# Optimization experiments

Hardware: AMD Instinct MI355X
Metric: run time of the kernel (lower is better)

## Reference

```python
import jax, jax.numpy as jnp
import numpy as np

B, L, D, H, F = 4, 1024, 1024, 16, 4096
HD = D // H
EPS = 1e-5


def _xavier(key, shape):
    fan_in, fan_out = shape[1], shape[0]
    a = np.sqrt(6.0 / (fan_in + fan_out)).astype(np.float32)
    return jax.random.uniform(key, shape, jnp.float32, -a, a)


def setup_inputs() -> dict:
    key = jax.random.key(0)
    ks = jax.random.split(key, 8)
    x = jax.random.normal(ks[0], (B, L, D), jnp.float32)
    attn_mask = jnp.zeros((L, L), jnp.float32)
    return {
        "x": x,
        "attn_mask": attn_mask,
        "in_proj_w": _xavier(ks[1], (3 * D, D)),
        "in_proj_b": jnp.zeros((3 * D,), jnp.float32),
        "out_proj_w": _xavier(ks[2], (D, D)),
        "out_proj_b": jnp.zeros((D,), jnp.float32),
        "lin1_w": _xavier(ks[3], (F, D)),
        "lin1_b": jnp.zeros((F,), jnp.float32),
        "lin2_w": _xavier(ks[4], (D, F)),
        "lin2_b": jnp.zeros((D,), jnp.float32),
        "ln1_g": jnp.ones((D,), jnp.float32),
        "ln1_b": jnp.zeros((D,), jnp.float32),
        "ln2_g": jnp.ones((D,), jnp.float32),
        "ln2_b": jnp.zeros((D,), jnp.float32),
    }


def _layernorm(x, g, b):
    mu = jnp.mean(x, axis=-1, keepdims=True)
    var = jnp.mean(jnp.square(x - mu), axis=-1, keepdims=True)
    return (x - mu) * jax.lax.rsqrt(var + EPS) * g + b


def reference(x, attn_mask, in_proj_w, in_proj_b, out_proj_w, out_proj_b,
              lin1_w, lin1_b, lin2_w, lin2_b, ln1_g, ln1_b, ln2_g, ln2_b):
    # --- self-attention (need_weights=True, average_attn_weights=False) ---
    qkv = x @ in_proj_w.T + in_proj_b          # [B,L,3D]
    q, k, v = jnp.split(qkv, 3, axis=-1)
    q = q.reshape(B, L, H, HD).transpose(0, 2, 1, 3)  # [B,H,L,hd]
    k = k.reshape(B, L, H, HD).transpose(0, 2, 1, 3)
    v = v.reshape(B, L, H, HD).transpose(0, 2, 1, 3)
    scores = jnp.einsum('bhqd,bhkd->bhqk', q, k) / np.sqrt(HD).astype(np.float32)
    scores = scores + attn_mask                # additive [L,L] mask
    attn_w = jax.nn.softmax(scores, axis=-1)   # [B,H,L,L] materialized weights
    ctx = jnp.einsum('bhqk,bhkd->bhqd', attn_w, v)
    ctx = ctx.transpose(0, 2, 1, 3).reshape(B, L, D)
    attn_out = ctx @ out_proj_w.T + out_proj_b
    # --- norm_first=False residual blocks ---
    x = _layernorm(x + attn_out, ln1_g, ln1_b)
    ff = jax.nn.relu(x @ lin1_w.T + lin1_b) @ lin2_w.T + lin2_b
    x = _layernorm(x + ff, ln2_g, ln2_b)
    return (x, attn_w)
```

## Files before the change

kernel.cpp:

```cpp
#include <hip/hip_runtime.h>

#define Bq 4
#define Lq 1024
#define Dq 1024
#define Hq 16
#define HDq 64
#define Fq 4096
#define Mq (Bq*Lq)

typedef unsigned short u16;
using short8  = __attribute__((ext_vector_type(8))) short;
using floatx4 = __attribute__((ext_vector_type(4))) float;

__device__ __forceinline__ float b2f(u16 u) {
  union { unsigned int i; float f; } v; v.i = ((unsigned int)u) << 16; return v.f;
}
__device__ __forceinline__ u16 f2b(float f) {
  union { float f; unsigned int i; } v; v.f = f;
  unsigned int x = v.i;
  unsigned int r = x + 0x7fffu + ((x >> 16) & 1u);
  return (u16)(r >> 16);
}

__device__ __forceinline__ void split2(float v, u16& hi, u16& lo) {
  hi = f2b(v);
  lo = f2b(v - b2f(hi));
}

__device__ __forceinline__ void gl_lds16(const u16* g, u16* l) {
  __builtin_amdgcn_global_load_lds(
      (const __attribute__((address_space(1))) void*)g,
      (__attribute__((address_space(3))) void*)l, 16, 0, 0);
}

__launch_bounds__(256)
__global__ void cvt_f32_bf16(const float* __restrict__ s, u16* __restrict__ d, int n4) {
  const int i = (blockIdx.x * 256 + threadIdx.x) * 4;
  if (i < n4) {
    float4 v = *(const float4*)(s + i);
    ushort4 o;
    o.x = f2b(v.x); o.y = f2b(v.y); o.z = f2b(v.z); o.w = f2b(v.w);
    *(ushort4*)(d + i) = o;
  }
}

template<bool RELU, typename OutT>
__launch_bounds__(256)
__global__ void gemm_bt(const u16* __restrict__ A, int lda,
                        const u16* __restrict__ B, int ldb,
                        const float* __restrict__ bias,
                        OutT* __restrict__ C, int ldc,
                        int K) {
  __shared__ __align__(16) u16 As[128 * 32];
  __shared__ __align__(16) u16 Bs[128 * 32];
  const int tid  = threadIdx.x;
  const int m0   = blockIdx.y * 128;
  const int n0   = blockIdx.x * 128;
  const int lane = tid & 63;
  const int wave = tid >> 6;
  const int wm   = (wave >> 1) * 64;
  const int wn   = (wave & 1) * 64;
  const int lrow = lane & 15;
  const int lk   = (lane >> 4) * 8;

  const int c0 = tid, c1 = tid + 256;
  const int ar0 = c0 >> 2, ac0 = (c0 & 3) * 8;
  const int ar1 = c1 >> 2, ac1 = (c1 & 3) * 8;

  floatx4 acc[4][4] = {};

  for (int k0 = 0; k0 < K; k0 += 32) {
    gl_lds16(A + (size_t)(m0 + ar0) * lda + k0 + ac0, &As[c0 * 8]);
    gl_lds16(A + (size_t)(m0 + ar1) * lda + k0 + ac1, &As[c1 * 8]);
    gl_lds16(B + (size_t)(n0 + ar0) * ldb + k0 + ac0, &Bs[c0 * 8]);
    gl_lds16(B + (size_t)(n0 + ar1) * ldb + k0 + ac1, &Bs[c1 * 8]);
    __syncthreads();

    short8 af[4], bf[4];
#pragma unroll
    for (int t = 0; t < 4; ++t) {
      af[t] = *(const short8*)&As[(wm + t * 16 + lrow) * 32 + lk];
      bf[t] = *(const short8*)&Bs[(wn + t * 16 + lrow) * 32 + lk];
    }
#pragma unroll
    for (int i = 0; i < 4; ++i)
#pragma unroll
      for (int j = 0; j < 4; ++j)
        acc[i][j] = __builtin_amdgcn_mfma_f32_16x16x32_bf16(af[i], bf[j], acc[i][j], 0, 0, 0);
    __syncthreads();
  }

#pragma unroll
  for (int i = 0; i < 4; ++i) {
    const int row = m0 + wm + i * 16 + (lane >> 4) * 4;
#pragma unroll
    for (int j = 0; j < 4; ++j) {
      const int col = n0 + wn + j * 16 + lrow;
      const float bv = bias[col];
#pragma unroll
      for (int r = 0; r < 4; ++r) {
        float v = acc[i][j][r] + bv;
        if (RELU) v = v > 0.f ? v : 0.f;
        if constexpr (sizeof(OutT) == 4) C[(size_t)(row + r) * ldc + col] = v;
        else                             C[(size_t)(row + r) * ldc + col] = f2b(v);
      }
    }
  }
}

__launch_bounds__(256)
__global__ void transpose_v(const float* __restrict__ qkv, u16* __restrict__ vt) {
  __shared__ __align__(16) float t[64][65];
  const int kt = blockIdx.x;
  const int h  = blockIdx.y;
  const int b  = blockIdx.z;
  const int tid = threadIdx.x;
#pragma unroll
  for (int i = 0; i < 16; ++i) {
    int e = i * 256 + tid;
    int kk = e >> 6, d = e & 63;
    t[kk][d] = qkv[((size_t)(b * Lq + kt * 64 + kk)) * (3 * Dq) + 2 * Dq + h * HDq + d];
  }
  __syncthreads();
#pragma unroll
  for (int i = 0; i < 16; ++i) {
    int e = i * 256 + tid;
    int drow = e >> 6, kcol = e & 63;
    vt[(((size_t)(b * Hq + h)) * HDq + drow) * Lq + kt * 64 + kcol] = f2b(t[kcol][drow]);
  }
}

__launch_bounds__(256)
__global__ void split_k(const float* __restrict__ qkv,
                        u16* __restrict__ kh, u16* __restrict__ kl) {
  const int gid = blockIdx.x * 256 + threadIdx.x;
  const int oct = gid & 7;
  const int l   = (gid >> 3) & 1023;
  const int h   = (gid >> 13) & 15;
  const int b   = gid >> 17;
  const float* src = qkv + ((size_t)(b * Lq + l)) * (3 * Dq) + Dq + h * HDq + oct * 8;
  float4 a = *(const float4*)src;
  float4 c = *(const float4*)(src + 4);
  float v[8] = {a.x, a.y, a.z, a.w, c.x, c.y, c.z, c.w};
  short8 hi, lo;
#pragma unroll
  for (int j = 0; j < 8; ++j) {
    u16 hh, ll; split2(v[j], hh, ll);
    hi[j] = (short)hh; lo[j] = (short)ll;
  }
  const size_t off = (((size_t)(b * Hq + h)) * Lq + l) * HDq + oct * 8;
  *(short8*)(kh + off) = hi;
  *(short8*)(kl + off) = lo;
}

__device__ __forceinline__ int sw_idx(int m, int c) {
  return m * 1024 + (c ^ ((m & 3) * 8));
}

__device__ __forceinline__ void load_split8(const float* p, short8& hi, short8& lo) {
  float4 a = *(const float4*)p;
  float4 b = *(const float4*)(p + 4);
  float v[8] = {a.x, a.y, a.z, a.w, b.x, b.y, b.z, b.w};
#pragma unroll
  for (int j = 0; j < 8; ++j) {
    u16 h, l; split2(v[j], h, l);
    hi[j] = (short)h; lo[j] = (short)l;
  }
}

__launch_bounds__(256)
__global__ void attn_kernel(const float* __restrict__ qkv,
                            const u16* __restrict__ kh,
                            const u16* __restrict__ kl,
                            const u16* __restrict__ vt,
                            const float* __restrict__ mask,
                            float* __restrict__ attn_w,
                            u16* __restrict__ ctx) {
  __shared__ __align__(16) float S[16 * 1024];
  const int qt  = blockIdx.x;
  const int h   = blockIdx.y;
  const int b   = blockIdx.z;
  const int tid = threadIdx.x;
  const int lane = tid & 63, wave = tid >> 6;
  const int lrow = lane & 15, quad = lane >> 4;
  const int q0 = qt * 16;

  const float* qbase = qkv + ((size_t)(b * Lq + q0 + lrow)) * (3 * Dq) + h * HDq + quad * 8;
  short8 aqh0, aql0, aqh1, aql1;
  load_split8(qbase,      aqh0, aql0);
  load_split8(qbase + 32, aqh1, aql1);

  const u16* khb = kh + (((size_t)(b * Hq + h)) * Lq) * HDq + quad * 8;
  const u16* klb = kl + (((size_t)(b * Hq + h)) * Lq) * HDq + quad * 8;
  for (int i = 0; i < 16; ++i) {
    const int n0 = wave * 256 + i * 16;
    const u16* kbh = khb + (size_t)(n0 + lrow) * HDq;
    const u16* kbl = klb + (size_t)(n0 + lrow) * HDq;
    short8 kh0 = *(const short8*)kbh;
    short8 kh1 = *(const short8*)(kbh + 32);
    short8 kl0 = *(const short8*)kbl;
    short8 kl1 = *(const short8*)(kbl + 32);
    floatx4 sc = {};
    sc = __builtin_amdgcn_mfma_f32_16x16x32_bf16(aqh0, kh0, sc, 0, 0, 0);
    sc = __builtin_amdgcn_mfma_f32_16x16x32_bf16(aqh0, kl0, sc, 0, 0, 0);
    sc = __builtin_amdgcn_mfma_f32_16x16x32_bf16(aql0, kh0, sc, 0, 0, 0);
    sc = __builtin_amdgcn_mfma_f32_16x16x32_bf16(aqh1, kh1, sc, 0, 0, 0);
    sc = __builtin_amdgcn_mfma_f32_16x16x32_bf16(aqh1, kl1, sc, 0, 0, 0);
    sc = __builtin_amdgcn_mfma_f32_16x16x32_bf16(aql1, kh1, sc, 0, 0, 0);
#pragma unroll
    for (int r = 0; r < 4; ++r)
      S[sw_idx(quad * 4 + r, n0 + lrow)] = sc[r] * 0.125f;
  }
  __syncthreads();

  const int row = tid >> 4, idx = tid & 15;
  const float* mrow = mask + (size_t)(q0 + row) * Lq;
  float mx = -1e30f;
#pragma unroll
  for (int j = 0; j < 16; ++j) {
    const int c = idx * 4 + j * 64;
    float* sp = &S[sw_idx(row, c)];
    float4 v4 = *(const float4*)sp;
    float4 m4 = *(const float4*)(mrow + c);
    v4.x += m4.x; v4.y += m4.y; v4.z += m4.z; v4.w += m4.w;
    *(float4*)sp = v4;
    mx = fmaxf(mx, fmaxf(fmaxf(v4.x, v4.y), fmaxf(v4.z, v4.w)));
  }
#pragma unroll
  for (int s = 1; s < 16; s <<= 1) mx = fmaxf(mx, __shfl_xor(mx, s, 16));
  float sum = 0.f;
#pragma unroll
  for (int j = 0; j < 16; ++j) {
    const int c = idx * 4 + j * 64;
    float* sp = &S[sw_idx(row, c)];
    float4 v4 = *(const float4*)sp;
    float4 p;
    p.x = __expf(v4.x - mx); p.y = __expf(v4.y - mx);
    p.z = __expf(v4.z - mx); p.w = __expf(v4.w - mx);
    *(float4*)sp = p;
    sum += (p.x + p.y) + (p.z + p.w);
  }
#pragma unroll
  for (int s = 1; s < 16; s <<= 1) sum += __shfl_xor(sum, s, 16);
  const float scl = 1.f / sum;

  float* wrow = attn_w + (((size_t)(b * Hq + h)) * Lq + q0 + row) * Lq;
#pragma unroll
  for (int j = 0; j < 16; ++j) {
    const int c = idx * 4 + j * 64;
    float* sp = &S[sw_idx(row, c)];
    float4 p = *(const float4*)sp;
    p.x *= scl; p.y *= scl; p.z *= scl; p.w *= scl;
    *(float4*)sp = p;
    *(float4*)(wrow + c) = p;
  }
  __syncthreads();

  const u16* vbase = vt + ((((size_t)(b * Hq + h)) * HDq) + wave * 16 + lrow) * Lq + quad * 8;
  floatx4 o = {};
  for (int kc = 0; kc < Lq; kc += 32) {
    const float* ps = &S[sw_idx(lrow, kc + quad * 8)];
    float4 p0 = *(const float4*)ps;
    float4 p1 = *(const float4*)(ps + 4);
    short8 ap;
    ap[0] = (short)f2b(p0.x); ap[1] = (short)f2b(p0.y);
    ap[2] = (short)f2b(p0.z); ap[3] = (short)f2b(p0.w);
    ap[4] = (short)f2b(p1.x); ap[5] = (short)f2b(p1.y);
    ap[6] = (short)f2b(p1.z); ap[7] = (short)f2b(p1.w);
    short8 bv = *(const short8*)(vbase + kc);
    o = __builtin_amdgcn_mfma_f32_16x16x32_bf16(ap, bv, o, 0, 0, 0);
  }
#pragma unroll
  for (int r = 0; r < 4; ++r) {
    const int qrow = q0 + quad * 4 + r;
    ctx[((size_t)(b * Lq) + qrow) * Dq + h * HDq + wave * 16 + lrow] = f2b(o[r]);
  }
}

template<typename OutT>
__launch_bounds__(256)
__global__ void add_ln(const u16* __restrict__ a, const u16* __restrict__ res,
                       const float* __restrict__ g, const float* __restrict__ be,
                       OutT* __restrict__ out) {
  const int rowi = blockIdx.x;
  const int tid = threadIdx.x;
  const u16* pa = a   + (size_t)rowi * Dq + tid * 4;
  const u16* pr = res + (size_t)rowi * Dq + tid * 4;
  ushort4 va = *(const ushort4*)pa;
  ushort4 vr = *(const ushort4*)pr;
  float v[4];
  float s = 0.f, s2 = 0.f;
#pragma unroll
  for (int j = 0; j < 4; ++j) {
    float x = b2f(((const u16*)&va)[j]) + b2f(((const u16*)&vr)[j]);
    v[j] = x; s += x; s2 += x * x;
  }
#pragma unroll
  for (int m = 1; m < 64; m <<= 1) { s += __shfl_xor(s, m, 64); s2 += __shfl_xor(s2, m, 64); }
  __shared__ float rs[4], rs2[4];
  const int wave = tid >> 6, lane = tid & 63;
  if (lane == 0) { rs[wave] = s; rs2[wave] = s2; }
  __syncthreads();
  s  = rs[0] + rs[1] + rs[2] + rs[3];
  s2 = rs2[0] + rs2[1] + rs2[2] + rs2[3];
  const float mean = s * (1.f / Dq);
  const float var  = s2 * (1.f / Dq) - mean * mean;
  const float rstd = rsqrtf(var + 1e-5f);
  float4 vg = *(const float4*)(g + tid * 4);
  float4 vb = *(const float4*)(be + tid * 4);
  float y0 = (v[0] - mean) * rstd * vg.x + vb.x;
  float y1 = (v[1] - mean) * rstd * vg.y + vb.y;
  float y2 = (v[2] - mean) * rstd * vg.z + vb.z;
  float y3 = (v[3] - mean) * rstd * vg.w + vb.w;
  if constexpr (sizeof(OutT) == 4) {
    float4 o = {y0, y1, y2, y3};
    *(float4*)(out + (size_t)rowi * Dq + tid * 4) = o;
  } else {
    ushort4 o;
    ((u16*)&o)[0] = f2b(y0); ((u16*)&o)[1] = f2b(y1);
    ((u16*)&o)[2] = f2b(y2); ((u16*)&o)[3] = f2b(y3);
    *(ushort4*)(out + (size_t)rowi * Dq + tid * 4) = o;
  }
}

extern "C" void kernel_launch(void* const* d_in, const int* in_sizes, int n_in,
                              void* d_out, int out_size, void* d_ws, size_t ws_size,
                              hipStream_t stream) {
  const float* x    = (const float*)d_in[0];
  const float* mask = (const float*)d_in[1];
  const float* win  = (const float*)d_in[2];
  const float* bin  = (const float*)d_in[3];
  const float* wo   = (const float*)d_in[4];
  const float* bo   = (const float*)d_in[5];
  const float* w1   = (const float*)d_in[6];
  const float* b1   = (const float*)d_in[7];
  const float* w2   = (const float*)d_in[8];
  const float* b2   = (const float*)d_in[9];
  const float* g1   = (const float*)d_in[10];
  const float* be1  = (const float*)d_in[11];
  const float* g2   = (const float*)d_in[12];
  const float* be2  = (const float*)d_in[13];

  float* out0  = (float*)d_out;
  float* attnw = out0 + (size_t)Bq * Lq * Dq;

  u16*   ws   = (u16*)d_ws;
  u16*   xb   = ws;
  float* qkvf = (float*)(ws + (size_t)4194304);
  u16*   vtb  = ws + (size_t)29360128;
  u16*   ctx  = ws + (size_t)33554432;
  u16*   aout = ws + (size_t)37748736;
  u16*   winb = ws + (size_t)41943040;
  u16*   wob  = ws + (size_t)45088768;
  u16*   w1b  = ws + (size_t)46137344;
  u16*   w2b  = ws + (size_t)50331648;
  u16*   y1   = aout;
  u16*   h1   = ws + (size_t)4194304;
  u16*   ff   = ctx;
  u16*   khb  = w1b;
  u16*   klb  = w2b;

  cvt_f32_bf16<<<4194304 / 1024, 256, 0, stream>>>(x,   xb,   4194304);
  cvt_f32_bf16<<<3145728 / 1024, 256, 0, stream>>>(win, winb, 3145728);

  gemm_bt<false, float><<<dim3(3 * Dq / 128, Mq / 128), 256, 0, stream>>>(
      xb, Dq, winb, Dq, bin, qkvf, 3 * Dq, Dq);
  transpose_v<<<dim3(16, Hq, Bq), 256, 0, stream>>>(qkvf, vtb);
  split_k<<<524288 / 256, 256, 0, stream>>>(qkvf, khb, klb);
  attn_kernel<<<dim3(Lq / 16, Hq, Bq), 256, 0, stream>>>(qkvf, khb, klb, vtb, mask, attnw, ctx);
  cvt_f32_bf16<<<1048576 / 1024, 256, 0, stream>>>(wo,  wob,  1048576);
  cvt_f32_bf16<<<4194304 / 1024, 256, 0, stream>>>(w1,  w1b,  4194304);
  cvt_f32_bf16<<<4194304 / 1024, 256, 0, stream>>>(w2,  w2b,  4194304);
  gemm_bt<false, u16><<<dim3(Dq / 128, Mq / 128), 256, 0, stream>>>(
      ctx, Dq, wob, Dq, bo, aout, Dq, Dq);
  add_ln<u16><<<Mq, 256, 0, stream>>>(xb, aout, g1, be1, y1);
  gemm_bt<true, u16><<<dim3(Fq / 128, Mq / 128), 256, 0, stream>>>(
      y1, Dq, w1b, Dq, b1, h1, Fq, Dq);
  gemm_bt<false, u16><<<dim3(Dq / 128, Mq / 128), 256, 0, stream>>>(
      h1, Fq, w2b, Fq, b2, ff, Dq, Fq);
  add_ln<float><<<Mq, 256, 0, stream>>>(y1, ff, g2, be2, out0);
}
```

Baseline: 787.2 us.

## Keep attention scores in registers, store bf16 probs in LDS, use 512 threads

The attention kernel now runs 8 waves per block and keeps the QK^T scores in registers. Softmax max and sum are reduced across waves through small shared arrays, so the fp32 scores no longer make several round trips through LDS. Probabilities are written to LDS once as bf16 with an XOR swizzle, shrinking LDS use so more blocks fit per CU. The PV product is split into two K halves whose partial results are combined through shared memory. Block indices are also remapped so neighbouring blocks touch different heads, at the cost of the extra reduction syncs and more registers per thread.

```diff
diff --git a/kernel.cpp b/kernel.cpp
--- a/kernel.cpp
+++ b/kernel.cpp
@@ -153,8 +153,8 @@
   *(short8*)(kl + off) = lo;
 }
 
-__device__ __forceinline__ int sw_idx(int m, int c) {
-  return m * 1024 + (c ^ ((m & 3) * 8));
+__device__ __forceinline__ int ps_idx(int row, int col) {
+  return row * 1024 + ((((col >> 3) ^ (row & 7)) << 3) | (col & 7));
 }
 
 __device__ __forceinline__ void load_split8(const float* p, short8& hi, short8& lo) {
@@ -168,7 +168,7 @@
   }
 }
 
-__launch_bounds__(256)
+__launch_bounds__(512, 4)
 __global__ void attn_kernel(const float* __restrict__ qkv,
                             const u16* __restrict__ kh,
                             const u16* __restrict__ kl,
@@ -176,11 +176,16 @@
                             const float* __restrict__ mask,
                             float* __restrict__ attn_w,
                             u16* __restrict__ ctx) {
-  __shared__ __align__(16) float S[16 * 1024];
-  const int qt  = blockIdx.x;
-  const int h   = blockIdx.y;
-  const int b   = blockIdx.z;
-  const int tid = threadIdx.x;
+  __shared__ __align__(16) u16 Ps[16 * 1024];
+  __shared__ float redmax[8][16];
+  __shared__ float redsum[8][16];
+  __shared__ float Pp[4][16][17];
+
+  int lid = (int)blockIdx.x + ((int)blockIdx.y << 6) + ((int)blockIdx.z << 10);
+  lid = (lid & 7) * 512 + (lid >> 3);
+  const int qt = lid & 63, h = (lid >> 6) & 15, b = lid >> 10;
+  const int bh = b * Hq + h;
+  const int tid  = threadIdx.x;
   const int lane = tid & 63, wave = tid >> 6;
   const int lrow = lane & 15, quad = lane >> 4;
   const int q0 = qt * 16;
@@ -190,90 +195,115 @@
   load_split8(qbase,      aqh0, aql0);
   load_split8(qbase + 32, aqh1, aql1);
 
-  const u16* khb = kh + (((size_t)(b * Hq + h)) * Lq) * HDq + quad * 8;
-  const u16* klb = kl + (((size_t)(b * Hq + h)) * Lq) * HDq + quad * 8;
-  for (int i = 0; i < 16; ++i) {
-    const int n0 = wave * 256 + i * 16;
+  const u16* khb = kh + ((size_t)bh * Lq) * HDq + quad * 8;
+  const u16* klb = kl + ((size_t)bh * Lq) * HDq + quad * 8;
+  floatx4 sc[8];
+#pragma unroll
+  for (int i = 0; i < 8; ++i) {
+    const int n0 = wave * 128 + i * 16;
     const u16* kbh = khb + (size_t)(n0 + lrow) * HDq;
     const u16* kbl = klb + (size_t)(n0 + lrow) * HDq;
-    short8 kh0 = *(const short8*)kbh;
-    short8 kh1 = *(const short8*)(kbh + 32);
-    short8 kl0 = *(const short8*)kbl;
-    short8 kl1 = *(const short8*)(kbl + 32);
-    floatx4 sc = {};
-    sc = __builtin_amdgcn_mfma_f32_16x16x32_bf16(aqh0, kh0, sc, 0, 0, 0);
-    sc = __builtin_amdgcn_mfma_f32_16x16x32_bf16(aqh0, kl0, sc, 0, 0, 0);
-    sc = __builtin_amdgcn_mfma_f32_16x16x32_bf16(aql0, kh0, sc, 0, 0, 0);
-    sc = __builtin_amdgcn_mfma_f32_16x16x32_bf16(aqh1, kh1, sc, 0, 0, 0);
-    sc = __builtin_amdgcn_mfma_f32_16x16x32_bf16(aqh1, kl1, sc, 0, 0, 0);
-    sc = __builtin_amdgcn_mfma_f32_16x16x32_bf16(aql1, kh1, sc, 0, 0, 0);
-#pragma unroll
-    for (int r = 0; r < 4; ++r)
-      S[sw_idx(quad * 4 + r, n0 + lrow)] = sc[r] * 0.125f;
-  }
-  __syncthreads();
-
-  const int row = tid >> 4, idx = tid & 15;
-  const float* mrow = mask + (size_t)(q0 + row) * Lq;
-  float mx = -1e30f;
-#pragma unroll
-  for (int j = 0; j < 16; ++j) {
-    const int c = idx * 4 + j * 64;
-    float* sp = &S[sw_idx(row, c)];
-    float4 v4 = *(const float4*)sp;
-    float4 m4 = *(const float4*)(mrow + c);
-    v4.x += m4.x; v4.y += m4.y; v4.z += m4.z; v4.w += m4.w;
-    *(float4*)sp = v4;
-    mx = fmaxf(mx, fmaxf(fmaxf(v4.x, v4.y), fmaxf(v4.z, v4.w)));
-  }
-#pragma unroll
-  for (int s = 1; s < 16; s <<= 1) mx = fmaxf(mx, __shfl_xor(mx, s, 16));
-  float sum = 0.f;
-#pragma unroll
-  for (int j = 0; j < 16; ++j) {
-    const int c = idx * 4 + j * 64;
-    float* sp = &S[sw_idx(row, c)];
-    float4 v4 = *(const float4*)sp;
-    float4 p;
-    p.x = __expf(v4.x - mx); p.y = __expf(v4.y - mx);
-    p.z = __expf(v4.z - mx); p.w = __expf(v4.w - mx);
-    *(float4*)sp = p;
-    sum += (p.x + p.y) + (p.z + p.w);
-  }
-#pragma unroll
-  for (int s = 1; s < 16; s <<= 1) sum += __shfl_xor(sum, s, 16);
-  const float scl = 1.f / sum;
-
-  float* wrow = attn_w + (((size_t)(b * Hq + h)) * Lq + q0 + row) * Lq;
-#pragma unroll
-  for (int j = 0; j < 16; ++j) {
-    const int c = idx * 4 + j * 64;
-    float* sp = &S[sw_idx(row, c)];
-    float4 p = *(const float4*)sp;
-    p.x *= scl; p.y *= scl; p.z *= scl; p.w *= scl;
-    *(float4*)sp = p;
-    *(float4*)(wrow + c) = p;
-  }
-  __syncthreads();
-
-  const u16* vbase = vt + ((((size_t)(b * Hq + h)) * HDq) + wave * 16 + lrow) * Lq + quad * 8;
+    short8 k0h = *(const short8*)kbh;
+    short8 k1h = *(const short8*)(kbh + 32);
+    short8 k0l = *(const short8*)kbl;
+    short8 k1l = *(const short8*)(kbl + 32);
+    floatx4 s = {};
+    s = __builtin_amdgcn_mfma_f32_16x16x32_bf16(aqh0, k0h, s, 0, 0, 0);
+    s = __builtin_amdgcn_mfma_f32_16x16x32_bf16(aqh0, k0l, s, 0, 0, 0);
+    s = __builtin_amdgcn_mfma_f32_16x16x32_bf16(aql0, k0h, s, 0, 0, 0);
+    s = __builtin_amdgcn_mfma_f32_16x16x32_bf16(aqh1, k1h, s, 0, 0, 0);
+    s = __builtin_amdgcn_mfma_f32_16x16x32_bf16(aqh1, k1l, s, 0, 0, 0);
+    s = __builtin_amdgcn_mfma_f32_16x16x32_bf16(aql1, k1h, s, 0, 0, 0);
+    sc[i] = s;
+  }
+
+  const float* mbase = mask + (size_t)(q0 + quad * 4) * Lq + wave * 128 + lrow;
+  float mx[4] = {-1e30f, -1e30f, -1e30f, -1e30f};
+#pragma unroll
+  for (int i = 0; i < 8; ++i)
+#pragma unroll
+    for (int r = 0; r < 4; ++r) {
+      float v = sc[i][r] * 0.125f + mbase[(size_t)r * Lq + i * 16];
+      sc[i][r] = v;
+      mx[r] = fmaxf(mx[r], v);
+    }
+#pragma unroll
+  for (int s = 1; s < 16; s <<= 1)
+#pragma unroll
+    for (int r = 0; r < 4; ++r) mx[r] = fmaxf(mx[r], __shfl_xor(mx[r], s, 16));
+  if (lrow == 0) {
+#pragma unroll
+    for (int r = 0; r < 4; ++r) redmax[wave][quad * 4 + r] = mx[r];
+  }
+  __syncthreads();
+  float M[4];
+#pragma unroll
+  for (int r = 0; r < 4; ++r) {
+    float m = redmax[0][quad * 4 + r];
+#pragma unroll
+    for (int w = 1; w < 8; ++w) m = fmaxf(m, redmax[w][quad * 4 + r]);
+    M[r] = m;
+  }
+
+  float sm[4] = {0.f, 0.f, 0.f, 0.f};
+#pragma unroll
+  for (int i = 0; i < 8; ++i)
+#pragma unroll
+    for (int r = 0; r < 4; ++r) {
+      float p = __expf(sc[i][r] - M[r]);
+      sc[i][r] = p;
+      sm[r] += p;
+    }
+#pragma unroll
+  for (int s = 1; s < 16; s <<= 1)
+#pragma unroll
+    for (int r = 0; r < 4; ++r) sm[r] += __shfl_xor(sm[r], s, 16);
+  if (lrow == 0) {
+#pragma unroll
+    for (int r = 0; r < 4; ++r) redsum[wave][quad * 4 + r] = sm[r];
+  }
+  __syncthreads();
+  float scl[4];
+#pragma unroll
+  for (int r = 0; r < 4; ++r) {
+    float t = redsum[0][quad * 4 + r];
+#pragma unroll
+    for (int w = 1; w < 8; ++w) t += redsum[w][quad * 4 + r];
+    scl[r] = 1.f / t;
+  }
+
+  float* wbase = attn_w + ((size_t)bh * Lq + q0 + quad * 4) * Lq + wave * 128 + lrow;
+#pragma unroll
+  for (int i = 0; i < 8; ++i)
+#pragma unroll
+    for (int r = 0; r < 4; ++r) {
+      float w = sc[i][r] * scl[r];
+      wbase[(size_t)r * Lq + i * 16] = w;
+      Ps[ps_idx(quad * 4 + r, wave * 128 + i * 16 + lrow)] = f2b(w);
+    }
+  __syncthreads();
+
+  const int dstrip = (wave & 3) * 16;
+  const int khalf  = (wave >> 2) * 512;
+  const u16* vbase = vt + ((size_t)bh * HDq + dstrip + lrow) * Lq + khalf + quad * 8;
   floatx4 o = {};
-  for (int kc = 0; kc < Lq; kc += 32) {
-    const float* ps = &S[sw_idx(lrow, kc + quad * 8)];
-    float4 p0 = *(const float4*)ps;
-    float4 p1 = *(const float4*)(ps + 4);
-    short8 ap;
-    ap[0] = (short)f2b(p0.x); ap[1] = (short)f2b(p0.y);
-    ap[2] = (short)f2b(p0.z); ap[3] = (short)f2b(p0.w);
-    ap[4] = (short)f2b(p1.x); ap[5] = (short)f2b(p1.y);
-    ap[6] = (short)f2b(p1.z); ap[7] = (short)f2b(p1.w);
+#pragma unroll
+  for (int kc = 0; kc < 512; kc += 32) {
+    short8 ap = *(const short8*)&Ps[ps_idx(lrow, khalf + kc + quad * 8)];
     short8 bv = *(const short8*)(vbase + kc);
     o = __builtin_amdgcn_mfma_f32_16x16x32_bf16(ap, bv, o, 0, 0, 0);
   }
-#pragma unroll
-  for (int r = 0; r < 4; ++r) {
-    const int qrow = q0 + quad * 4 + r;
-    ctx[((size_t)(b * Lq) + qrow) * Dq + h * HDq + wave * 16 + lrow] = f2b(o[r]);
+  if (wave >= 4) {
+#pragma unroll
+    for (int r = 0; r < 4; ++r) Pp[wave - 4][quad * 4 + r][lrow] = o[r];
+  }
+  __syncthreads();
+  if (wave < 4) {
+#pragma unroll
+    for (int r = 0; r < 4; ++r) {
+      float v = o[r] + Pp[wave][quad * 4 + r][lrow];
+      ctx[((size_t)(b * Lq) + q0 + quad * 4 + r) * Dq + h * HDq + dstrip + lrow] = f2b(v);
+    }
   }
 }
 
@@ -367,7 +397,7 @@
       xb, Dq, winb, Dq, bin, qkvf, 3 * Dq, Dq);
   transpose_v<<<dim3(16, Hq, Bq), 256, 0, stream>>>(qkvf, vtb);
   split_k<<<524288 / 256, 256, 0, stream>>>(qkvf, khb, klb);
-  attn_kernel<<<dim3(Lq / 16, Hq, Bq), 256, 0, stream>>>(qkvf, khb, klb, vtb, mask, attnw, ctx);
+  attn_kernel<<<dim3(Lq / 16, Hq, Bq), 512, 0, stream>>>(qkvf, khb, klb, vtb, mask, attnw, ctx);
   cvt_f32_bf16<<<1048576 / 1024, 256, 0, stream>>>(wo,  wob,  1048576);
   cvt_f32_bf16<<<4194304 / 1024, 256, 0, stream>>>(w1,  w1b,  4194304);
   cvt_f32_bf16<<<4194304 / 1024, 256, 0, stream>>>(w2,  w2b,  4194304);
```

Result: faster. 765.0 us (-2.8%).
